# Performance work log

Measured on AMD Instinct MI355X. Metric: run time of the kernel, lower is better.

The kernel has to match this reference:

```python
import jax, jax.numpy as jnp
import numpy as np

B, C, W, F, NC = 512, 12, 4, 512, 4  # batch, leads, windows(=4, hardcoded by conv0), features, classes


def setup_inputs() -> dict:
    key = jax.random.key(0)
    ks = jax.random.split(key, 16)
    g = lambda i, shape, s=1.0: jax.random.normal(ks[i], shape, jnp.float32) * s
    return {
        "x": g(0, (B, C, W, F)),
        # GRU (PyTorch layout: W_ih [3F,F], W_hh [3F,F], gate order r,z,n)
        "gru_wih": g(1, (3 * F, F), 0.03),
        "gru_whh": g(2, (3 * F, F), 0.03),
        "gru_bih": jnp.zeros((3 * F,), jnp.float32),
        "gru_bhh": jnp.zeros((3 * F,), jnp.float32),
        # GraphLearning 1x1 convs (squeezed kernels); positive biases keep adj nondegenerate
        "conv0_w": g(3, (W,), 0.5), "conv0_b": jnp.float32(0.1),
        "conv1_w": g(4, (F,), 0.05), "conv1_b": jnp.float32(0.1),
        "conv2_w": g(5, (C * C, C), 0.3),
        "conv2_b": 0.1 + 0.05 * jnp.abs(g(6, (C * C,))),
        # GCN stack
        "gcn_w": g(7, (2, F, F), 0.04), "gcn_b": jnp.zeros((2, F), jnp.float32),
        # classifier head (jax [in,out] layout); BN in eval mode
        "fc1_w": g(8, (C * F, 512), 0.02), "fc1_b": jnp.zeros((512,), jnp.float32),
        "bn1_g": jnp.ones((512,), jnp.float32), "bn1_b": jnp.zeros((512,), jnp.float32),
        "bn1_m": 0.1 * g(9, (512,)), "bn1_v": 1.0 + 0.1 * jnp.abs(g(10, (512,))),
        "fc2_w": g(11, (512, 512), 0.04), "fc2_b": jnp.zeros((512,), jnp.float32),
        "bn2_g": jnp.ones((512,), jnp.float32), "bn2_b": jnp.zeros((512,), jnp.float32),
        "bn2_m": 0.1 * g(12, (512,)), "bn2_v": 1.0 + 0.1 * jnp.abs(g(13, (512,))),
        "fc3_w": g(14, (512, NC), 0.04), "fc3_b": jnp.zeros((NC,), jnp.float32),
    }


def reference(x, gru_wih, gru_whh, gru_bih, gru_bhh,
              conv0_w, conv0_b, conv1_w, conv1_b, conv2_w, conv2_b,
              gcn_w, gcn_b,
              fc1_w, fc1_b, bn1_g, bn1_b, bn1_m, bn1_v,
              fc2_w, fc2_b, bn2_g, bn2_b, bn2_m, bn2_v,
              fc3_w, fc3_b):
    b, c, w, f = x.shape
    # --- GRU over leads dim; each window slice starts from h0=0, so merge (batch, w) ---
    xs = x.transpose(0, 2, 1, 3).reshape(b * w, c, f)            # [N, C, F]
    xW = jnp.einsum('ntf,gf->ntg', xs, gru_wih) + gru_bih        # precompute input gates [N,C,3F]

    def step(h, xw_t):
        hg = h @ gru_whh.T + gru_bhh
        xr, xz, xn = jnp.split(xw_t, 3, axis=-1)
        hr, hz, hn = jnp.split(hg, 3, axis=-1)
        r = jax.nn.sigmoid(xr + hr)
        z = jax.nn.sigmoid(xz + hz)
        n = jnp.tanh(xn + r * hn)
        h = (1.0 - z) * n + z * h
        return h, h

    _, hs = jax.lax.scan(step, jnp.zeros((b * w, f), x.dtype), xW.transpose(1, 0, 2))
    gru_out = hs.transpose(1, 0, 2).reshape(b, w, c, f).transpose(0, 2, 1, 3)  # [B,C,W,F]

    # --- GraphLearning: 1x1 convs -> 12x12 adjacency -> normalized Laplacian -> Chebyshev K=4 ---
    g0 = gru_out.transpose(0, 2, 1, 3)                               # [B,W,C,F]
    y = jax.nn.relu(jnp.einsum('bwcf,w->bcf', g0, conv0_w) + conv0_b)  # [B,C,F]
    y = jax.nn.relu(jnp.einsum('bcf,f->bc', y, conv1_w) + conv1_b)     # [B,C]
    y = jax.nn.relu(jnp.einsum('bc,kc->bk', y, conv2_w) + conv2_b)     # [B,C*C]
    a = jnp.mean(y.reshape(b, c, c), axis=0)
    adj = jax.nn.relu(a)
    degree = jnp.sum(adj, axis=1)
    adj_s = 0.5 * (adj + adj.T)
    d_hat = 1.0 / (jnp.sqrt(degree) + 1e-7)
    lap = d_hat[:, None] * (jnp.diag(degree) - adj_s) * d_hat[None, :]
    L0 = jnp.zeros_like(lap)
    L1 = lap
    L2 = 2.0 * lap @ L1 - L0
    L3 = 2.0 * lap @ L2 - L1
    cheb = jnp.stack([L0, L1, L2, L3], axis=0)                       # [4,C,C]

    # --- GCN stack with residuals (dropout is identity in eval) ---
    h = gru_out.transpose(0, 2, 1, 3)[:, :, None]                    # [B,W,1,C,F]
    tmp = h
    res = h
    for i in range(gcn_w.shape[0]):
        support = jnp.einsum('bwocf,fg->bwocg', h, gcn_w[i])
        out = jnp.einsum('wij,bwojf->bwoif', cheb, support) + gcn_b[i]
        h = jax.nn.relu(out) + res
        res = h
    h = tmp + h
    h = h[:, :, 0].sum(1).reshape(b, c * f)                          # [B, C*F]

    # --- classifier head (eval-mode BN, dropout identity) ---
    def bn(v, gmm, bt, m, var):
        return (v - m) / jnp.sqrt(var + 1e-5) * gmm + bt

    h = bn(jax.nn.leaky_relu(h @ fc1_w + fc1_b, 0.01), bn1_g, bn1_b, bn1_m, bn1_v)
    h = bn(jax.nn.leaky_relu(h @ fc2_w + fc2_b, 0.01), bn2_g, bn2_b, bn2_m, bn2_v)
    return h @ fc3_w + fc3_b
```

## Files before the change

kernel.cpp:

```cpp
#include <hip/hip_runtime.h>
#include <cmath>

constexpr int Bb  = 512;
constexpr int Cc  = 12;
constexpr int Ww  = 4;
constexpr int Ff  = 512;
constexpr int Nn  = Bb * Ww;
constexpr int Gg  = 3 * Ff;
constexpr int Mx  = Nn * Cc;

typedef __attribute__((ext_vector_type(8))) short bf16x8;
typedef __attribute__((ext_vector_type(4))) float f32x4;

__device__ __forceinline__ float sigm(float v) { return 1.f / (1.f + expf(-v)); }
__device__ __forceinline__ float b2f(ushort u) { union { float f; unsigned i; } v; v.i = ((unsigned)u) << 16; return v.f; }
__device__ __forceinline__ ushort f2b(float f) {
    union { float f; unsigned i; } v; v.f = f;
    unsigned r = v.i + 0x7FFFu + ((v.i >> 16) & 1u);
    return (ushort)(r >> 16);
}
__device__ __forceinline__ void async16(const ushort* g, ushort* l) {
    __builtin_amdgcn_global_load_lds(
        (const __attribute__((address_space(1))) unsigned int*)g,
        (__attribute__((address_space(3))) unsigned int*)l, 16, 0, 0);
}

__global__ __launch_bounds__(256) void mfma_gemm(
    const ushort* __restrict__ A, const ushort* __restrict__ Bt,
    float* __restrict__ Cf, ushort* __restrict__ Cb,
    const float* __restrict__ colBias,
    int N, int K, int kLen, int MN, int gridY)
{
    __shared__ ushort As[128 * 64], Bs[128 * 64];
    const int tid = threadIdx.x;
    const int ln = tid & 63, wv = tid >> 6;
    const int l = blockIdx.x;
    const int by = l % gridY, bx = l / gridY, bz = blockIdx.y;
    const int srow = ln >> 3;
    const int kslot = (ln & 7) ^ srow;
    const int rowA0 = by * 128 + wv * 32;
    const int rowB0 = bx * 128 + wv * 32;
    const ushort* ga = A  + (long)(rowA0 + srow) * K + bz * kLen + kslot * 8;
    const ushort* gb = Bt + (long)(rowB0 + srow) * K + bz * kLen + kslot * 8;
    ushort* la = As + wv * 32 * 64;
    ushort* lb = Bs + wv * 32 * 64;
    const int rbase = (wv >> 1) * 64, cbase = (wv & 1) * 64;
    const int mrow = ln & 15, quad = ln >> 4;

    f32x4 acc[4][4] = {};

    for (int kc = 0; kc < kLen; kc += 64) {
        #pragma unroll
        for (int i = 0; i < 4; ++i) {
            async16(ga + (long)(i * 8) * K, la + i * 8 * 64);
            async16(gb + (long)(i * 8) * K, lb + i * 8 * 64);
        }
        ga += 64; gb += 64;
        __syncthreads();
        #pragma unroll
        for (int s = 0; s < 2; ++s) {
            const int sw = (((s << 2) + quad) ^ (ln & 7)) << 3;
            bf16x8 af[4], bf[4];
            #pragma unroll
            for (int i = 0; i < 4; ++i)
                af[i] = *(const bf16x8*)(As + (rbase + i * 16 + mrow) * 64 + sw);
            #pragma unroll
            for (int j = 0; j < 4; ++j)
                bf[j] = *(const bf16x8*)(Bs + (cbase + j * 16 + mrow) * 64 + sw);
            #pragma unroll
            for (int i = 0; i < 4; ++i)
                #pragma unroll
                for (int j = 0; j < 4; ++j)
                    acc[i][j] = __builtin_amdgcn_mfma_f32_16x16x32_bf16(af[i], bf[j], acc[i][j], 0, 0, 0);
        }
        __syncthreads();
    }

    const int gr0 = by * 128 + rbase + quad * 4;
    const int gc0 = bx * 128 + cbase + mrow;
    if (Cb) {
        float cb[4] = {0.f, 0.f, 0.f, 0.f};
        if (colBias) {
            #pragma unroll
            for (int j = 0; j < 4; ++j) cb[j] = colBias[gc0 + j * 16];
        }
        #pragma unroll
        for (int i = 0; i < 4; ++i)
            #pragma unroll
            for (int r = 0; r < 4; ++r) {
                const int row = gr0 + i * 16 + r;
                #pragma unroll
                for (int j = 0; j < 4; ++j)
                    Cb[(long)row * N + gc0 + j * 16] = f2b(acc[i][j][r] + cb[j]);
            }
    } else {
        float* Co = Cf + (long)bz * MN;
        #pragma unroll
        for (int i = 0; i < 4; ++i)
            #pragma unroll
            for (int r = 0; r < 4; ++r) {
                const int row = gr0 + i * 16 + r;
                #pragma unroll
                for (int j = 0; j < 4; ++j)
                    Co[(long)row * N + gc0 + j * 16] = acc[i][j][r];
            }
    }
}

__global__ __launch_bounds__(256) void gru_fused(
    const ushort* __restrict__ hin, const ushort* __restrict__ whhB,
    const ushort* __restrict__ xw, const float* __restrict__ bhh,
    ushort* __restrict__ hout, ushort* __restrict__ G, int t)
{
    __shared__ ushort As[64 * 64], Bs[96 * 64];
    const int tid = threadIdx.x, ln = tid & 63, wv = tid >> 6;
    const int l = blockIdx.x;
    const int mb = l & 31, fb = l >> 5;
    const int srow = ln >> 3, kslot = (ln & 7) ^ srow;
    const int mrow = ln & 15, quad = ln >> 4;
    f32x4 acc[6] = {};
    const ushort* ha = hin + (long)(mb * 64) * 512;

    for (int kc = 0; kc < 512; kc += 64) {
        #pragma unroll
        for (int a = 0; a < 2; ++a) {
            const int r0 = (wv * 2 + a) * 8;
            async16(ha + (long)(r0 + srow) * 512 + kc + kslot * 8, As + r0 * 64);
        }
        #pragma unroll
        for (int b8 = 0; b8 < 3; ++b8) {
            const int lr0 = (wv * 3 + b8) * 8;
            const int lr = lr0 + srow;
            const int g = lr >> 5, fc = lr & 31;
            async16(whhB + (long)(g * 512 + fb * 32 + fc) * 512 + kc + kslot * 8, Bs + lr0 * 64);
        }
        __syncthreads();
        #pragma unroll
        for (int s = 0; s < 2; ++s) {
            const int sw = (((s << 2) + quad) ^ (ln & 7)) << 3;
            const bf16x8 a = *(const bf16x8*)(As + (wv * 16 + mrow) * 64 + sw);
            #pragma unroll
            for (int jt = 0; jt < 6; ++jt) {
                const bf16x8 b = *(const bf16x8*)(Bs + (jt * 16 + mrow) * 64 + sw);
                acc[jt] = __builtin_amdgcn_mfma_f32_16x16x32_bf16(a, b, acc[jt], 0, 0, 0);
            }
        }
        __syncthreads();
    }

    #pragma unroll
    for (int ft = 0; ft < 2; ++ft) {
        const int f = fb * 32 + ft * 16 + mrow;
        const float bhn = bhh[1024 + f];
        #pragma unroll
        for (int r = 0; r < 4; ++r) {
            const int n = mb * 64 + wv * 16 + quad * 4 + r;
            const long xbase = (long)(n * 12 + t) * 1536 + f;
            const float xr = b2f(xw[xbase]);
            const float xz = b2f(xw[xbase + 512]);
            const float xn = b2f(xw[xbase + 1024]);
            const float rr = sigm(xr + acc[ft][r]);
            const float zz = sigm(xz + acc[2 + ft][r]);
            const float nv = tanhf(xn + rr * (acc[4 + ft][r] + bhn));
            const float hv = (1.f - zz) * nv + zz * b2f(hin[(long)n * 512 + f]);
            const ushort hb = f2b(hv);
            hout[(long)n * 512 + f] = hb;
            G[(long)(n * 12 + t) * 512 + f] = hb;
        }
    }
}

__global__ __launch_bounds__(256) void cvt_x(const float* __restrict__ x, ushort* __restrict__ xb)
{
    const int idx = blockIdx.x * 256 + threadIdx.x;
    const int m = idx >> 6, f8 = (idx & 63) << 3;
    const int n = m / 12, c = m - n * 12;
    const int b = n >> 2, w = n & 3;
    const float* src = x + (((b * 12 + c) * 4 + w) << 9) + f8;
    const float4 a = *(const float4*)src, q = *(const float4*)(src + 4);
    uint4 o;
    o.x = (unsigned)f2b(a.x) | ((unsigned)f2b(a.y) << 16);
    o.y = (unsigned)f2b(a.z) | ((unsigned)f2b(a.w) << 16);
    o.z = (unsigned)f2b(q.x) | ((unsigned)f2b(q.y) << 16);
    o.w = (unsigned)f2b(q.z) | ((unsigned)f2b(q.w) << 16);
    *(uint4*)(xb + (m << 9) + f8) = o;
}

__global__ __launch_bounds__(256) void cvt_mat(const float* __restrict__ src, ushort* __restrict__ dst)
{
    const int idx = blockIdx.x * 256 + threadIdx.x;
    const int e = idx << 3;
    const float4 a = *(const float4*)(src + e), q = *(const float4*)(src + e + 4);
    uint4 o;
    o.x = (unsigned)f2b(a.x) | ((unsigned)f2b(a.y) << 16);
    o.y = (unsigned)f2b(a.z) | ((unsigned)f2b(a.w) << 16);
    o.z = (unsigned)f2b(q.x) | ((unsigned)f2b(q.y) << 16);
    o.w = (unsigned)f2b(q.z) | ((unsigned)f2b(q.w) << 16);
    *(uint4*)(dst + e) = o;
}

__global__ __launch_bounds__(256) void tcvt(const float* __restrict__ src, ushort* __restrict__ dst, int R, int C)
{
    __shared__ float t[32][33];
    const int c0 = blockIdx.x * 32, r0 = blockIdx.y * 32;
    const int cx = threadIdx.x & 31, ry = threadIdx.x >> 5;
    #pragma unroll
    for (int k = 0; k < 4; ++k) t[ry + k * 8][cx] = src[(long)(r0 + ry + k * 8) * C + c0 + cx];
    __syncthreads();
    #pragma unroll
    for (int k = 0; k < 4; ++k) dst[(long)(c0 + ry + k * 8) * R + r0 + cx] = f2b(t[cx][ry + k * 8]);
}

__global__ __launch_bounds__(256) void bias_combo(
    const float* __restrict__ bih, const float* __restrict__ bhh, float* __restrict__ out)
{
    const int i = blockIdx.x * 256 + threadIdx.x;
    out[i] = bih[i] + (i < 1024 ? bhh[i] : 0.f);
}

__global__ __launch_bounds__(256) void conv01(
    const ushort* __restrict__ G, const float* __restrict__ w0, const float* __restrict__ b0,
    const float* __restrict__ w1, const float* __restrict__ b1, float* __restrict__ y2)
{
    const int row = (blockIdx.x * 256 + threadIdx.x) >> 6;
    const int lane = threadIdx.x & 63;
    const int b = row / 12, c = row - 12 * b;
    const float w00 = w0[0], w01 = w0[1], w02 = w0[2], w03 = w0[3], bb = b0[0];
    const ushort* gp = G + ((long)(b * 4) * 12 + c) * 512;
    float s = 0.f;
    for (int f = lane; f < 512; f += 64) {
        const float v = bb + b2f(gp[f]) * w00 + b2f(gp[6144 + f]) * w01
                      + b2f(gp[12288 + f]) * w02 + b2f(gp[18432 + f]) * w03;
        s += fmaxf(v, 0.f) * w1[f];
    }
    #pragma unroll
    for (int off = 32; off; off >>= 1) s += __shfl_down(s, off);
    if (lane == 0) y2[row] = fmaxf(s + b1[0], 0.f);
}

__global__ __launch_bounds__(256) void conv2_mean(
    const float* __restrict__ y2, const float* __restrict__ w2,
    const float* __restrict__ b2, float* __restrict__ adjr)
{
    __shared__ float red[256];
    const int k = blockIdx.x, tid = threadIdx.x;
    float wk[12];
    #pragma unroll
    for (int c = 0; c < 12; ++c) wk[c] = w2[k * 12 + c];
    const float bias = b2[k];
    float part = 0.f;
    for (int b = tid; b < Bb; b += 256) {
        const float* yb = y2 + b * 12;
        float s = bias;
        #pragma unroll
        for (int c = 0; c < 12; ++c) s += yb[c] * wk[c];
        part += fmaxf(s, 0.f);
    }
    red[tid] = part; __syncthreads();
    for (int off = 128; off; off >>= 1) { if (tid < off) red[tid] += red[tid + off]; __syncthreads(); }
    if (tid == 0) adjr[k] = red[0] * (1.f / Bb);
}

__global__ __launch_bounds__(256) void build_cheb(const float* __restrict__ adjr, float* __restrict__ cheb)
{
    __shared__ float adj[12][12], deg[12], dhat[12], lap[12][12], T2[12][12];
    const int tid = threadIdx.x;
    if (tid < 144) adj[tid / 12][tid % 12] = fmaxf(adjr[tid], 0.f);
    __syncthreads();
    if (tid < 12) {
        float s = 0.f;
        for (int j = 0; j < 12; ++j) s += adj[tid][j];
        deg[tid] = s; dhat[tid] = 1.f / (sqrtf(s) + 1e-7f);
    }
    __syncthreads();
    if (tid < 144) {
        const int i = tid / 12, j = tid % 12;
        const float as = 0.5f * (adj[i][j] + adj[j][i]);
        lap[i][j] = dhat[i] * ((i == j ? deg[i] : 0.f) - as) * dhat[j];
    }
    __syncthreads();
    if (tid < 144) {
        const int i = tid / 12, j = tid % 12;
        float s = 0.f;
        for (int kk = 0; kk < 12; ++kk) s += lap[i][kk] * lap[kk][j];
        T2[i][j] = 2.f * s;
    }
    __syncthreads();
    if (tid < 144) {
        const int i = tid / 12, j = tid % 12;
        float s = 0.f;
        for (int kk = 0; kk < 12; ++kk) s += lap[i][kk] * T2[kk][j];
        cheb[tid] = 0.f;
        cheb[144 + tid] = lap[i][j];
        cheb[288 + tid] = T2[i][j];
        cheb[432 + tid] = 2.f * s - lap[i][j];
    }
}

__global__ __launch_bounds__(256) void gcn_epi1(
    const ushort* __restrict__ S, const float* __restrict__ cheb,
    const float* __restrict__ gcnb, const ushort* __restrict__ G,
    ushort* __restrict__ H1)
{
    __shared__ float ch[576];
    const int tid = threadIdx.x;
    for (int i = tid; i < 576; i += 256) ch[i] = cheb[i];
    __syncthreads();
    const int idx = blockIdx.x * 256 + tid;
    const int f = idx & 511, bc = idx >> 9;
    const int b = bc / 12, c = bc - 12 * b;
    const float bias = gcnb[f];
    #pragma unroll
    for (int w = 0; w < 4; ++w) {
        float o = bias;
        const ushort* Sr = S + ((b * 4 + w) * 12) * 512 + f;
        const float* cw = ch + w * 144 + c * 12;
        #pragma unroll
        for (int j = 0; j < 12; ++j) o += cw[j] * b2f(Sr[j * 512]);
        const int gi = ((b * 4 + w) * 12 + c) * 512 + f;
        H1[gi] = f2b(fmaxf(o, 0.f) + b2f(G[gi]));
    }
}

__global__ __launch_bounds__(256) void gcn_epi2(
    const ushort* __restrict__ S, const float* __restrict__ cheb,
    const float* __restrict__ gcnb, const ushort* __restrict__ G,
    const ushort* __restrict__ H1, ushort* __restrict__ pooled)
{
    __shared__ float ch[576];
    const int tid = threadIdx.x;
    for (int i = tid; i < 576; i += 256) ch[i] = cheb[i];
    __syncthreads();
    const int idx = blockIdx.x * 256 + tid;
    const int f = idx & 511, bc = idx >> 9;
    const int b = bc / 12, c = bc - 12 * b;
    const float bias = gcnb[f];
    float acc = 0.f;
    #pragma unroll
    for (int w = 0; w < 4; ++w) {
        float o = bias;
        const ushort* Sr = S + ((b * 4 + w) * 12) * 512 + f;
        const float* cw = ch + w * 144 + c * 12;
        #pragma unroll
        for (int j = 0; j < 12; ++j) o += cw[j] * b2f(Sr[j * 512]);
        const int gi = ((b * 4 + w) * 12 + c) * 512 + f;
        acc += fmaxf(o, 0.f) + b2f(H1[gi]) + b2f(G[gi]);
    }
    pooled[idx] = f2b(acc);
}

__global__ __launch_bounds__(256) void fc_epi(
    const float* __restrict__ part, int nsplit, const float* __restrict__ bias,
    const float* __restrict__ g, const float* __restrict__ be,
    const float* __restrict__ mu, const float* __restrict__ var,
    ushort* __restrict__ outb, float* __restrict__ outf)
{
    const int idx = blockIdx.x * 256 + threadIdx.x;
    const int c = idx & 511;
    float s = bias[c];
    for (int k = 0; k < nsplit; ++k) s += part[k * 262144 + idx];
    s = s >= 0.f ? s : 0.01f * s;
    s = (s - mu[c]) * rsqrtf(var[c] + 1e-5f) * g[c] + be[c];
    if (outb) outb[idx] = f2b(s); else outf[idx] = s;
}

__global__ __launch_bounds__(256) void fc3_kernel(
    const float* __restrict__ z2, const float* __restrict__ w3,
    const float* __restrict__ b3, float* __restrict__ out)
{
    const int idx = blockIdx.x * 256 + threadIdx.x;
    const int m = idx >> 2, nc = idx & 3;
    float s = b3[nc];
    const float* zr = z2 + m * 512;
    for (int k = 0; k < 512; ++k) s += zr[k] * w3[k * 4 + nc];
    out[idx] = s;
}

extern "C" void kernel_launch(void* const* d_in, const int* in_sizes, int n_in,
                              void* d_out, int out_size, void* d_ws, size_t ws_size,
                              hipStream_t stream)
{
    (void)in_sizes; (void)n_in; (void)out_size; (void)ws_size;
    const float* x    = (const float*)d_in[0];
    const float* wih  = (const float*)d_in[1];
    const float* whh  = (const float*)d_in[2];
    const float* bih  = (const float*)d_in[3];
    const float* bhh  = (const float*)d_in[4];
    const float* c0w  = (const float*)d_in[5];
    const float* c0b  = (const float*)d_in[6];
    const float* c1w  = (const float*)d_in[7];
    const float* c1b  = (const float*)d_in[8];
    const float* c2w  = (const float*)d_in[9];
    const float* c2b  = (const float*)d_in[10];
    const float* gcnw = (const float*)d_in[11];
    const float* gcnb = (const float*)d_in[12];
    const float* f1w  = (const float*)d_in[13];
    const float* f1b  = (const float*)d_in[14];
    const float* bn1g = (const float*)d_in[15];
    const float* bn1b = (const float*)d_in[16];
    const float* bn1m = (const float*)d_in[17];
    const float* bn1v = (const float*)d_in[18];
    const float* f2w  = (const float*)d_in[19];
    const float* f2b_ = (const float*)d_in[20];
    const float* bn2g = (const float*)d_in[21];
    const float* bn2b = (const float*)d_in[22];
    const float* bn2m = (const float*)d_in[23];
    const float* bn2v = (const float*)d_in[24];
    const float* f3w  = (const float*)d_in[25];
    const float* f3b  = (const float*)d_in[26];

    char* W = (char*)d_ws;
    ushort* xw     = (ushort*)(W + 0);
    ushort* S      = (ushort*)(W + 0);
    ushort* H1     = (ushort*)(W + 33554432);
    ushort* xb     = (ushort*)(W + 75497472);
    ushort* pooled = (ushort*)(W + 75497472);
    float*  z1p    = (float*)(W + 81788928);
    float*  z2p    = (float*)(W + 81788928);
    ushort* z1b    = (ushort*)(W + 98566144);
    float*  z2     = (float*)(W + 99090432);
    float*  y2     = (float*)(W + 100139008);
    float*  adjr   = (float*)(W + 100163584);
    float*  chebb  = (float*)(W + 100164608);
    ushort* G      = (ushort*)(W + 100663296);
    ushort* h0     = (ushort*)(W + 125829120);
    ushort* h1     = (ushort*)(W + 127926272);
    ushort* wihB   = (ushort*)(W + 130023424);
    ushort* whhB   = (ushort*)(W + 131596288);
    ushort* gw0    = (ushort*)(W + 133169152);
    ushort* gw1    = (ushort*)(W + 133693440);
    ushort* f1t    = (ushort*)(W + 134217728);
    ushort* f2t    = (ushort*)(W + 140509184);
    float*  biasc  = (float*)(W + 141033472);

    hipMemsetAsync(h0, 0, (size_t)Nn * Ff * sizeof(ushort), stream);
    cvt_x<<<(Mx * 64) / 256, 256, 0, stream>>>(x, xb);
    cvt_mat<<<(Gg * Ff / 8) / 256, 256, 0, stream>>>(wih, wihB);
    cvt_mat<<<(Gg * Ff / 8) / 256, 256, 0, stream>>>(whh, whhB);
    bias_combo<<<6, 256, 0, stream>>>(bih, bhh, biasc);
    tcvt<<<dim3(16, 16), 256, 0, stream>>>(gcnw, gw0, 512, 512);
    tcvt<<<dim3(16, 16), 256, 0, stream>>>(gcnw + 262144, gw1, 512, 512);
    tcvt<<<dim3(16, 192), 256, 0, stream>>>(f1w, f1t, 6144, 512);
    tcvt<<<dim3(16, 16), 256, 0, stream>>>(f2w, f2t, 512, 512);

    mfma_gemm<<<dim3(2304, 1), 256, 0, stream>>>(
        xb, wihB, nullptr, xw, biasc, Gg, Ff, Ff, 0, 192);

    ushort* hp = h0; ushort* hq = h1;
    for (int t = 0; t < Cc; ++t) {
        gru_fused<<<512, 256, 0, stream>>>(hp, whhB, xw, bhh, hq, G, t);
        ushort* tmp = hp; hp = hq; hq = tmp;
    }

    conv01<<<(Bb * Cc * 64) / 256, 256, 0, stream>>>(G, c0w, c0b, c1w, c1b, y2);
    conv2_mean<<<Cc * Cc, 256, 0, stream>>>(y2, c2w, c2b, adjr);
    build_cheb<<<1, 256, 0, stream>>>(adjr, chebb);

    mfma_gemm<<<dim3(768, 1), 256, 0, stream>>>(
        G, gw0, nullptr, S, nullptr, Ff, Ff, Ff, 0, 192);
    gcn_epi1<<<(Bb * Cc * Ff) / 256, 256, 0, stream>>>(S, chebb, gcnb, G, H1);

    mfma_gemm<<<dim3(768, 1), 256, 0, stream>>>(
        H1, gw1, nullptr, S, nullptr, Ff, Ff, Ff, 0, 192);
    gcn_epi2<<<(Bb * Cc * Ff) / 256, 256, 0, stream>>>(S, chebb, gcnb + Ff, G, H1, pooled);

    mfma_gemm<<<dim3(16, 16), 256, 0, stream>>>(
        pooled, f1t, z1p, nullptr, nullptr, 512, Cc * Ff, 384, 262144, 4);
    fc_epi<<<1024, 256, 0, stream>>>(z1p, 16, f1b, bn1g, bn1b, bn1m, bn1v, z1b, nullptr);
    mfma_gemm<<<dim3(16, 4), 256, 0, stream>>>(
        z1b, f2t, z2p, nullptr, nullptr, 512, 512, 128, 262144, 4);
    fc_epi<<<1024, 256, 0, stream>>>(z2p, 4, f2b_, bn2g, bn2b, bn2m, bn2v, nullptr, z2);
    fc3_kernel<<<(Bb * 4) / 256, 256, 0, stream>>>(z2, f3w, f3b, (float*)d_out);
}
```

Baseline: 522.7 us.

## Fuse GRU input projection into recurrent step kernel and merge prep kernels

Removes the separate input-gate GEMM and its large bf16 xw buffer. Each GRU step kernel now also computes x_t·W_ih with MFMA alongside h·W_hh and adds the biases in the epilogue. The MFMA operand order is swapped so each lane holds four consecutive columns, which allows vectorized epilogue stores. Weight conversion/transpose kernels and the conv2/cheb kernels are merged to cut launch count. The cost is doubled MFMA and LDS work inside the serial 12-step recurrence, and conv2 now runs as a single block.

```diff
diff --git a/kernel.cpp b/kernel.cpp
--- a/kernel.cpp
+++ b/kernel.cpp
@@ -71,102 +71,120 @@
             for (int i = 0; i < 4; ++i)
                 #pragma unroll
                 for (int j = 0; j < 4; ++j)
-                    acc[i][j] = __builtin_amdgcn_mfma_f32_16x16x32_bf16(af[i], bf[j], acc[i][j], 0, 0, 0);
+                    acc[i][j] = __builtin_amdgcn_mfma_f32_16x16x32_bf16(bf[j], af[i], acc[i][j], 0, 0, 0);
         }
         __syncthreads();
     }
 
-    const int gr0 = by * 128 + rbase + quad * 4;
-    const int gc0 = bx * 128 + cbase + mrow;
+    const int gr0 = by * 128 + rbase + mrow;
+    const int gc0 = bx * 128 + cbase + quad * 4;
     if (Cb) {
-        float cb[4] = {0.f, 0.f, 0.f, 0.f};
-        if (colBias) {
-            #pragma unroll
-            for (int j = 0; j < 4; ++j) cb[j] = colBias[gc0 + j * 16];
-        }
-        #pragma unroll
-        for (int i = 0; i < 4; ++i)
-            #pragma unroll
-            for (int r = 0; r < 4; ++r) {
-                const int row = gr0 + i * 16 + r;
-                #pragma unroll
-                for (int j = 0; j < 4; ++j)
-                    Cb[(long)row * N + gc0 + j * 16] = f2b(acc[i][j][r] + cb[j]);
+        #pragma unroll
+        for (int i = 0; i < 4; ++i) {
+            const long rowoff = (long)(gr0 + i * 16) * N;
+            #pragma unroll
+            for (int j = 0; j < 4; ++j) {
+                float c0 = 0.f, c1 = 0.f, c2 = 0.f, c3 = 0.f;
+                if (colBias) {
+                    const float4 cb4 = *(const float4*)(colBias + gc0 + j * 16);
+                    c0 = cb4.x; c1 = cb4.y; c2 = cb4.z; c3 = cb4.w;
+                }
+                union { ushort u[4]; uint2 v; } pk;
+                pk.u[0] = f2b(acc[i][j][0] + c0);
+                pk.u[1] = f2b(acc[i][j][1] + c1);
+                pk.u[2] = f2b(acc[i][j][2] + c2);
+                pk.u[3] = f2b(acc[i][j][3] + c3);
+                *(uint2*)&Cb[rowoff + gc0 + j * 16] = pk.v;
             }
+        }
     } else {
         float* Co = Cf + (long)bz * MN;
         #pragma unroll
-        for (int i = 0; i < 4; ++i)
-            #pragma unroll
-            for (int r = 0; r < 4; ++r) {
-                const int row = gr0 + i * 16 + r;
-                #pragma unroll
-                for (int j = 0; j < 4; ++j)
-                    Co[(long)row * N + gc0 + j * 16] = acc[i][j][r];
-            }
+        for (int i = 0; i < 4; ++i) {
+            const long rowoff = (long)(gr0 + i * 16) * N;
+            #pragma unroll
+            for (int j = 0; j < 4; ++j)
+                *(f32x4*)&Co[rowoff + gc0 + j * 16] = acc[i][j];
+        }
     }
 }
 
 __global__ __launch_bounds__(256) void gru_fused(
-    const ushort* __restrict__ hin, const ushort* __restrict__ whhB,
-    const ushort* __restrict__ xw, const float* __restrict__ bhh,
+    const ushort* __restrict__ hin, const ushort* __restrict__ xb,
+    const ushort* __restrict__ whhB, const ushort* __restrict__ wihB,
+    const float* __restrict__ bih, const float* __restrict__ bhh,
     ushort* __restrict__ hout, ushort* __restrict__ G, int t)
 {
-    __shared__ ushort As[64 * 64], Bs[96 * 64];
+    __shared__ ushort Ah[64 * 64], Ax[64 * 64], Bh[96 * 64], Bx[96 * 64];
     const int tid = threadIdx.x, ln = tid & 63, wv = tid >> 6;
-    const int l = blockIdx.x;
-    const int mb = l & 31, fb = l >> 5;
+    const int mb = blockIdx.x & 31, fb = blockIdx.x >> 5;
     const int srow = ln >> 3, kslot = (ln & 7) ^ srow;
     const int mrow = ln & 15, quad = ln >> 4;
-    f32x4 acc[6] = {};
-    const ushort* ha = hin + (long)(mb * 64) * 512;
+    f32x4 aH[6] = {}, aX[6] = {};
+    const ushort* hrow = hin + (long)(mb * 64) * 512;
 
     for (int kc = 0; kc < 512; kc += 64) {
         #pragma unroll
         for (int a = 0; a < 2; ++a) {
             const int r0 = (wv * 2 + a) * 8;
-            async16(ha + (long)(r0 + srow) * 512 + kc + kslot * 8, As + r0 * 64);
+            async16(hrow + (long)(r0 + srow) * 512 + kc + kslot * 8, Ah + r0 * 64);
+            async16(xb + ((long)(mb * 64 + r0 + srow) * 12 + t) * 512 + kc + kslot * 8, Ax + r0 * 64);
         }
         #pragma unroll
         for (int b8 = 0; b8 < 3; ++b8) {
             const int lr0 = (wv * 3 + b8) * 8;
             const int lr = lr0 + srow;
             const int g = lr >> 5, fc = lr & 31;
-            async16(whhB + (long)(g * 512 + fb * 32 + fc) * 512 + kc + kslot * 8, Bs + lr0 * 64);
+            const long wr = (long)(g * 512 + fb * 32 + fc) * 512 + kc + kslot * 8;
+            async16(whhB + wr, Bh + lr0 * 64);
+            async16(wihB + wr, Bx + lr0 * 64);
         }
         __syncthreads();
         #pragma unroll
         for (int s = 0; s < 2; ++s) {
             const int sw = (((s << 2) + quad) ^ (ln & 7)) << 3;
-            const bf16x8 a = *(const bf16x8*)(As + (wv * 16 + mrow) * 64 + sw);
+            const bf16x8 ah = *(const bf16x8*)(Ah + (wv * 16 + mrow) * 64 + sw);
+            const bf16x8 ax = *(const bf16x8*)(Ax + (wv * 16 + mrow) * 64 + sw);
             #pragma unroll
             for (int jt = 0; jt < 6; ++jt) {
-                const bf16x8 b = *(const bf16x8*)(Bs + (jt * 16 + mrow) * 64 + sw);
-                acc[jt] = __builtin_amdgcn_mfma_f32_16x16x32_bf16(a, b, acc[jt], 0, 0, 0);
+                const bf16x8 bh = *(const bf16x8*)(Bh + (jt * 16 + mrow) * 64 + sw);
+                aH[jt] = __builtin_amdgcn_mfma_f32_16x16x32_bf16(bh, ah, aH[jt], 0, 0, 0);
             }
+            #pragma unroll
+            for (int jt = 0; jt < 6; ++jt) {
+                const bf16x8 bx2 = *(const bf16x8*)(Bx + (jt * 16 + mrow) * 64 + sw);
+                aX[jt] = __builtin_amdgcn_mfma_f32_16x16x32_bf16(bx2, ax, aX[jt], 0, 0, 0);
+            }
         }
         __syncthreads();
     }
 
+    const int n = mb * 64 + wv * 16 + mrow;
     #pragma unroll
     for (int ft = 0; ft < 2; ++ft) {
-        const int f = fb * 32 + ft * 16 + mrow;
-        const float bhn = bhh[1024 + f];
+        const int f0 = fb * 32 + ft * 16 + quad * 4;
+        const float4 bir = *(const float4*)(bih + f0);
+        const float4 biz = *(const float4*)(bih + 512 + f0);
+        const float4 bin = *(const float4*)(bih + 1024 + f0);
+        const float4 bhr = *(const float4*)(bhh + f0);
+        const float4 bhz = *(const float4*)(bhh + 512 + f0);
+        const float4 bhn = *(const float4*)(bhh + 1024 + f0);
+        union { ushort u[4]; uint2 v; } hp;
+        hp.v = *(const uint2*)(hin + (long)n * 512 + f0);
+        const float br[4] = {bir.x + bhr.x, bir.y + bhr.y, bir.z + bhr.z, bir.w + bhr.w};
+        const float bz[4] = {biz.x + bhz.x, biz.y + bhz.y, biz.z + bhz.z, biz.w + bhz.w};
+        const float bn_i[4] = {bin.x, bin.y, bin.z, bin.w};
+        const float bn_h[4] = {bhn.x, bhn.y, bhn.z, bhn.w};
+        union { ushort u[4]; uint2 v; } o;
         #pragma unroll
         for (int r = 0; r < 4; ++r) {
-            const int n = mb * 64 + wv * 16 + quad * 4 + r;
-            const long xbase = (long)(n * 12 + t) * 1536 + f;
-            const float xr = b2f(xw[xbase]);
-            const float xz = b2f(xw[xbase + 512]);
-            const float xn = b2f(xw[xbase + 1024]);
-            const float rr = sigm(xr + acc[ft][r]);
-            const float zz = sigm(xz + acc[2 + ft][r]);
-            const float nv = tanhf(xn + rr * (acc[4 + ft][r] + bhn));
-            const float hv = (1.f - zz) * nv + zz * b2f(hin[(long)n * 512 + f]);
-            const ushort hb = f2b(hv);
-            hout[(long)n * 512 + f] = hb;
-            G[(long)(n * 12 + t) * 512 + f] = hb;
-        }
+            const float rr = sigm(aH[ft][r] + aX[ft][r] + br[r]);
+            const float zz = sigm(aH[2 + ft][r] + aX[2 + ft][r] + bz[r]);
+            const float nv = tanhf(aX[4 + ft][r] + bn_i[r] + rr * (aH[4 + ft][r] + bn_h[r]));
+            o.u[r] = f2b((1.f - zz) * nv + zz * b2f(hp.u[r]));
+        }
+        *(uint2*)&hout[(long)n * 512 + f0] = o.v;
+        *(uint2*)&G[(long)(n * 12 + t) * 512 + f0] = o.v;
     }
 }
 
@@ -186,36 +204,42 @@
     *(uint4*)(xb + (m << 9) + f8) = o;
 }
 
-__global__ __launch_bounds__(256) void cvt_mat(const float* __restrict__ src, ushort* __restrict__ dst)
-{
-    const int idx = blockIdx.x * 256 + threadIdx.x;
-    const int e = idx << 3;
-    const float4 a = *(const float4*)(src + e), q = *(const float4*)(src + e + 4);
+__global__ __launch_bounds__(256) void cvt_w2(
+    const float* __restrict__ wih, const float* __restrict__ whh,
+    ushort* __restrict__ wihB, ushort* __restrict__ whhB)
+{
+    int bx = blockIdx.x;
+    const float* s; ushort* d;
+    if (bx < 384) { s = wih; d = wihB; } else { s = whh; d = whhB; bx -= 384; }
+    const int e = (bx * 256 + threadIdx.x) << 3;
+    const float4 a = *(const float4*)(s + e), q = *(const float4*)(s + e + 4);
     uint4 o;
     o.x = (unsigned)f2b(a.x) | ((unsigned)f2b(a.y) << 16);
     o.y = (unsigned)f2b(a.z) | ((unsigned)f2b(a.w) << 16);
     o.z = (unsigned)f2b(q.x) | ((unsigned)f2b(q.y) << 16);
     o.w = (unsigned)f2b(q.z) | ((unsigned)f2b(q.w) << 16);
-    *(uint4*)(dst + e) = o;
-}
-
-__global__ __launch_bounds__(256) void tcvt(const float* __restrict__ src, ushort* __restrict__ dst, int R, int C)
-{
-    __shared__ float t[32][33];
-    const int c0 = blockIdx.x * 32, r0 = blockIdx.y * 32;
+    *(uint4*)(d + e) = o;
+}
+
+__global__ __launch_bounds__(256) void tcvt_all(
+    const float* __restrict__ gcnw, const float* __restrict__ f1w, const float* __restrict__ f2w,
+    ushort* __restrict__ gw0, ushort* __restrict__ gw1,
+    ushort* __restrict__ f1t, ushort* __restrict__ f2t)
+{
+    int by = blockIdx.y;
+    const float* src; ushort* dst; int R, C;
+    if (by < 16)       { src = gcnw;          dst = gw0; R = 512;  C = 512; }
+    else if (by < 32)  { src = gcnw + 262144; dst = gw1; R = 512;  C = 512; by -= 16; }
+    else if (by < 224) { src = f1w;           dst = f1t; R = 6144; C = 512; by -= 32; }
+    else               { src = f2w;           dst = f2t; R = 512;  C = 512; by -= 224; }
+    __shared__ float tl[32][33];
+    const int c0 = blockIdx.x * 32, r0 = by * 32;
     const int cx = threadIdx.x & 31, ry = threadIdx.x >> 5;
     #pragma unroll
-    for (int k = 0; k < 4; ++k) t[ry + k * 8][cx] = src[(long)(r0 + ry + k * 8) * C + c0 + cx];
-    __syncthreads();
-    #pragma unroll
-    for (int k = 0; k < 4; ++k) dst[(long)(c0 + ry + k * 8) * R + r0 + cx] = f2b(t[cx][ry + k * 8]);
-}
-
-__global__ __launch_bounds__(256) void bias_combo(
-    const float* __restrict__ bih, const float* __restrict__ bhh, float* __restrict__ out)
-{
-    const int i = blockIdx.x * 256 + threadIdx.x;
-    out[i] = bih[i] + (i < 1024 ? bhh[i] : 0.f);
+    for (int k = 0; k < 4; ++k) tl[ry + k * 8][cx] = src[(long)(r0 + ry + k * 8) * C + c0 + cx];
+    __syncthreads();
+    #pragma unroll
+    for (int k = 0; k < 4; ++k) dst[(long)(c0 + ry + k * 8) * R + r0 + cx] = f2b(tl[cx][ry + k * 8]);
 }
 
 __global__ __launch_bounds__(256) void conv01(
@@ -238,62 +262,57 @@
     if (lane == 0) y2[row] = fmaxf(s + b1[0], 0.f);
 }
 
-__global__ __launch_bounds__(256) void conv2_mean(
+__global__ __launch_bounds__(256) void conv2_cheb(
     const float* __restrict__ y2, const float* __restrict__ w2,
-    const float* __restrict__ b2, float* __restrict__ adjr)
-{
-    __shared__ float red[256];
-    const int k = blockIdx.x, tid = threadIdx.x;
-    float wk[12];
-    #pragma unroll
-    for (int c = 0; c < 12; ++c) wk[c] = w2[k * 12 + c];
-    const float bias = b2[k];
-    float part = 0.f;
-    for (int b = tid; b < Bb; b += 256) {
-        const float* yb = y2 + b * 12;
-        float s = bias;
-        #pragma unroll
-        for (int c = 0; c < 12; ++c) s += yb[c] * wk[c];
-        part += fmaxf(s, 0.f);
-    }
-    red[tid] = part; __syncthreads();
-    for (int off = 128; off; off >>= 1) { if (tid < off) red[tid] += red[tid + off]; __syncthreads(); }
-    if (tid == 0) adjr[k] = red[0] * (1.f / Bb);
-}
-
-__global__ __launch_bounds__(256) void build_cheb(const float* __restrict__ adjr, float* __restrict__ cheb)
-{
-    __shared__ float adj[12][12], deg[12], dhat[12], lap[12][12], T2[12][12];
+    const float* __restrict__ b2, float* __restrict__ cheb)
+{
+    __shared__ float ys[6144];
+    __shared__ float adj[144], deg[12], dhat[12], lap[144], T2[144];
     const int tid = threadIdx.x;
-    if (tid < 144) adj[tid / 12][tid % 12] = fmaxf(adjr[tid], 0.f);
+    for (int i = tid; i < 6144; i += 256) ys[i] = y2[i];
+    __syncthreads();
+    if (tid < 144) {
+        float wk[12];
+        #pragma unroll
+        for (int c = 0; c < 12; ++c) wk[c] = w2[tid * 12 + c];
+        const float bias = b2[tid];
+        float s = 0.f;
+        for (int b = 0; b < 512; ++b) {
+            float v = bias;
+            #pragma unroll
+            for (int c = 0; c < 12; ++c) v += ys[b * 12 + c] * wk[c];
+            s += fmaxf(v, 0.f);
+        }
+        adj[tid] = fmaxf(s * (1.f / 512.f), 0.f);
+    }
     __syncthreads();
     if (tid < 12) {
         float s = 0.f;
-        for (int j = 0; j < 12; ++j) s += adj[tid][j];
+        for (int j = 0; j < 12; ++j) s += adj[tid * 12 + j];
         deg[tid] = s; dhat[tid] = 1.f / (sqrtf(s) + 1e-7f);
     }
     __syncthreads();
     if (tid < 144) {
         const int i = tid / 12, j = tid % 12;
-        const float as = 0.5f * (adj[i][j] + adj[j][i]);
-        lap[i][j] = dhat[i] * ((i == j ? deg[i] : 0.f) - as) * dhat[j];
+        const float as = 0.5f * (adj[i * 12 + j] + adj[j * 12 + i]);
+        lap[tid] = dhat[i] * ((i == j ? deg[i] : 0.f) - as) * dhat[j];
     }
     __syncthreads();
     if (tid < 144) {
         const int i = tid / 12, j = tid % 12;
         float s = 0.f;
-        for (int kk = 0; kk < 12; ++kk) s += lap[i][kk] * lap[kk][j];
-        T2[i][j] = 2.f * s;
+        for (int kk = 0; kk < 12; ++kk) s += lap[i * 12 + kk] * lap[kk * 12 + j];
+        T2[tid] = 2.f * s;
     }
     __syncthreads();
     if (tid < 144) {
         const int i = tid / 12, j = tid % 12;
         float s = 0.f;
-        for (int kk = 0; kk < 12; ++kk) s += lap[i][kk] * T2[kk][j];
+        for (int kk = 0; kk < 12; ++kk) s += lap[i * 12 + kk] * T2[kk * 12 + j];
         cheb[tid] = 0.f;
-        cheb[144 + tid] = lap[i][j];
-        cheb[288 + tid] = T2[i][j];
-        cheb[432 + tid] = 2.f * s - lap[i][j];
+        cheb[144 + tid] = lap[tid];
+        cheb[288 + tid] = T2[tid];
+        cheb[432 + tid] = 2.f * s - lap[tid];
     }
 }
 
@@ -410,51 +429,39 @@
     const float* f3b  = (const float*)d_in[26];
 
     char* W = (char*)d_ws;
-    ushort* xw     = (ushort*)(W + 0);
-    ushort* S      = (ushort*)(W + 0);
-    ushort* H1     = (ushort*)(W + 33554432);
-    ushort* xb     = (ushort*)(W + 75497472);
-    ushort* pooled = (ushort*)(W + 75497472);
-    float*  z1p    = (float*)(W + 81788928);
-    float*  z2p    = (float*)(W + 81788928);
-    ushort* z1b    = (ushort*)(W + 98566144);
-    float*  z2     = (float*)(W + 99090432);
-    float*  y2     = (float*)(W + 100139008);
-    float*  adjr   = (float*)(W + 100163584);
-    float*  chebb  = (float*)(W + 100164608);
-    ushort* G      = (ushort*)(W + 100663296);
-    ushort* h0     = (ushort*)(W + 125829120);
-    ushort* h1     = (ushort*)(W + 127926272);
-    ushort* wihB   = (ushort*)(W + 130023424);
-    ushort* whhB   = (ushort*)(W + 131596288);
-    ushort* gw0    = (ushort*)(W + 133169152);
-    ushort* gw1    = (ushort*)(W + 133693440);
-    ushort* f1t    = (ushort*)(W + 134217728);
-    ushort* f2t    = (ushort*)(W + 140509184);
-    float*  biasc  = (float*)(W + 141033472);
+    ushort* xb     = (ushort*)(W + 0);
+    ushort* pooled = (ushort*)(W + 0);
+    float*  z1p    = (float*)(W + 8388608);
+    float*  z2p    = z1p;
+    ushort* G      = (ushort*)(W + 25165824);
+    ushort* S      = (ushort*)(W + 50331648);
+    ushort* H1     = (ushort*)(W + 75497472);
+    ushort* h0     = (ushort*)(W + 100663296);
+    ushort* h1     = (ushort*)(W + 102760448);
+    ushort* wihB   = (ushort*)(W + 104857600);
+    ushort* whhB   = (ushort*)(W + 106430464);
+    ushort* gw0    = (ushort*)(W + 108003328);
+    ushort* gw1    = (ushort*)(W + 108527616);
+    ushort* f1t    = (ushort*)(W + 109051904);
+    ushort* f2t    = (ushort*)(W + 115343360);
+    ushort* z1b    = (ushort*)(W + 115867648);
+    float*  z2     = (float*)(W + 116391936);
+    float*  y2     = (float*)(W + 117440512);
+    float*  chebb  = (float*)(W + 117465088);
 
     hipMemsetAsync(h0, 0, (size_t)Nn * Ff * sizeof(ushort), stream);
     cvt_x<<<(Mx * 64) / 256, 256, 0, stream>>>(x, xb);
-    cvt_mat<<<(Gg * Ff / 8) / 256, 256, 0, stream>>>(wih, wihB);
-    cvt_mat<<<(Gg * Ff / 8) / 256, 256, 0, stream>>>(whh, whhB);
-    bias_combo<<<6, 256, 0, stream>>>(bih, bhh, biasc);
-    tcvt<<<dim3(16, 16), 256, 0, stream>>>(gcnw, gw0, 512, 512);
-    tcvt<<<dim3(16, 16), 256, 0, stream>>>(gcnw + 262144, gw1, 512, 512);
-    tcvt<<<dim3(16, 192), 256, 0, stream>>>(f1w, f1t, 6144, 512);
-    tcvt<<<dim3(16, 16), 256, 0, stream>>>(f2w, f2t, 512, 512);
-
-    mfma_gemm<<<dim3(2304, 1), 256, 0, stream>>>(
-        xb, wihB, nullptr, xw, biasc, Gg, Ff, Ff, 0, 192);
+    cvt_w2<<<768, 256, 0, stream>>>(wih, whh, wihB, whhB);
+    tcvt_all<<<dim3(16, 240), 256, 0, stream>>>(gcnw, f1w, f2w, gw0, gw1, f1t, f2t);
 
     ushort* hp = h0; ushort* hq = h1;
     for (int t = 0; t < Cc; ++t) {
-        gru_fused<<<512, 256, 0, stream>>>(hp, whhB, xw, bhh, hq, G, t);
+        gru_fused<<<512, 256, 0, stream>>>(hp, xb, whhB, wihB, bih, bhh, hq, G, t);
         ushort* tmp = hp; hp = hq; hq = tmp;
     }
 
     conv01<<<(Bb * Cc * 64) / 256, 256, 0, stream>>>(G, c0w, c0b, c1w, c1b, y2);
-    conv2_mean<<<Cc * Cc, 256, 0, stream>>>(y2, c2w, c2b, adjr);
-    build_cheb<<<1, 256, 0, stream>>>(adjr, chebb);
+    conv2_cheb<<<1, 256, 0, stream>>>(y2, c2w, c2b, chebb);
 
     mfma_gemm<<<dim3(768, 1), 256, 0, stream>>>(
         G, gw0, nullptr, S, nullptr, Ff, Ff, Ff, 0, 192);
```

New measurement: 493.5 us. 5.6% less time.
